# Performance work log

Measured on AMD Instinct MI355X. Metric: run time of the kernel, lower is better.

Reference implementation:

```python
import jax, jax.numpy as jnp
import numpy as np

NEG_SLOPE = 0.2
N_GRAPHS = 32

def gat_conv(x, src, dst, W, attn_l, attn_r, bias):
    """DGL-style GATConv: returns [N, H, D]."""
    H, D = attn_l.shape
    N = x.shape[0]
    feat = (x @ W).reshape(N, H, D)                     # [N,H,D]
    el = jnp.sum(feat * attn_l[None], axis=-1)          # [N,H]
    er = jnp.sum(feat * attn_r[None], axis=-1)          # [N,H]
    e = jax.nn.leaky_relu(el[src] + er[dst], NEG_SLOPE) # [E,H]
    # edge softmax over incoming edges of each dst node
    emax = jax.ops.segment_max(e, dst, num_segments=N)
    emax = jnp.where(jnp.isfinite(emax), emax, 0.0)     # zero in-degree guard
    ex = jnp.exp(e - emax[dst])
    den = jax.ops.segment_sum(ex, dst, num_segments=N)
    alpha = ex / jnp.maximum(den[dst], 1e-9)            # [E,H]
    msg = alpha[:, :, None] * feat[src]                 # [E,H,D]
    rst = jax.ops.segment_sum(msg, dst, num_segments=N) # [N,H,D]
    return rst + bias.reshape(1, H, D)

def branch(x, src, dst, gid, W1, al1, ar1, b1, W2, al2, ar2, b2):
    h = jax.nn.relu(gat_conv(x, src, dst, W1, al1, ar1, b1))  # [N,10,64]
    h = h.sum(axis=1)                                          # [N,64]
    h = jax.nn.relu(gat_conv(h, src, dst, W2, al2, ar2, b2))  # [N,1,128]
    h = h[:, 0, :]                                             # [N,128]
    g = jax.ops.segment_max(h, gid, num_segments=N_GRAPHS)     # [B,128] max readout
    return jnp.where(jnp.isfinite(g), g, 0.0)

def reference(lig_x, lig_src, lig_dst, lig_gid, rec_x, rec_src, rec_dst, rec_gid,
              W1l, al1l, ar1l, b1l, W2l, al2l, ar2l, b2l,
              W1r, al1r, ar1r, b1r, W2r, al2r, ar2r, b2r,
              Wlin1, blin1, Wlin2, blin2):
    hlig = branch(lig_x, lig_src, lig_dst, lig_gid, W1l, al1l, ar1l, b1l, W2l, al2l, ar2l, b2l)
    hrec = branch(rec_x, rec_src, rec_dst, rec_gid, W1r, al1r, ar1r, b1r, W2r, al2r, ar2r, b2r)
    h = jnp.concatenate([hlig, hrec], axis=1)           # [B,256]
    h = jax.nn.relu(h @ Wlin1 + blin1)
    h = jax.nn.relu(h @ Wlin2 + blin2)
    return h.reshape(-1)

def setup_inputs() -> dict:
    key = jax.random.key(0)
    ks = jax.random.split(key, 24)
    Nl, El, Nr, Er = 20000, 160000, 40000, 400000
    d = {}
    d['lig_x'] = jax.random.normal(ks[0], (Nl, 64), jnp.float32)
    d['lig_src'] = jax.random.randint(ks[1], (El,), 0, Nl, jnp.int32)
    d['lig_dst'] = jax.random.randint(ks[2], (El,), 0, Nl, jnp.int32)
    d['lig_gid'] = jnp.sort(jax.random.randint(ks[3], (Nl,), 0, N_GRAPHS, jnp.int32))
    d['rec_x'] = jax.random.normal(ks[4], (Nr, 64), jnp.float32)
    d['rec_src'] = jax.random.randint(ks[5], (Er,), 0, Nr, jnp.int32)
    d['rec_dst'] = jax.random.randint(ks[6], (Er,), 0, Nr, jnp.int32)
    d['rec_gid'] = jnp.sort(jax.random.randint(ks[7], (Nr,), 0, N_GRAPHS, jnp.int32))
    s = 0.1
    d['W1l'] = jax.random.normal(ks[8], (64, 640), jnp.float32) * s
    d['al1l'] = jax.random.normal(ks[9], (10, 64), jnp.float32) * s
    d['ar1l'] = jax.random.normal(ks[10], (10, 64), jnp.float32) * s
    d['b1l'] = jnp.zeros((640,), jnp.float32)
    d['W2l'] = jax.random.normal(ks[11], (64, 128), jnp.float32) * s
    d['al2l'] = jax.random.normal(ks[12], (1, 128), jnp.float32) * s
    d['ar2l'] = jax.random.normal(ks[13], (1, 128), jnp.float32) * s
    d['b2l'] = jnp.zeros((128,), jnp.float32)
    d['W1r'] = jax.random.normal(ks[14], (64, 640), jnp.float32) * s
    d['al1r'] = jax.random.normal(ks[15], (10, 64), jnp.float32) * s
    d['ar1r'] = jax.random.normal(ks[16], (10, 64), jnp.float32) * s
    d['b1r'] = jnp.zeros((640,), jnp.float32)
    d['W2r'] = jax.random.normal(ks[17], (64, 128), jnp.float32) * s
    d['al2r'] = jax.random.normal(ks[18], (1, 128), jnp.float32) * s
    d['ar2r'] = jax.random.normal(ks[19], (1, 128), jnp.float32) * s
    d['b2r'] = jnp.zeros((128,), jnp.float32)
    d['Wlin1'] = jax.random.normal(ks[20], (256, 128), jnp.float32) * s
    d['blin1'] = jnp.zeros((128,), jnp.float32)
    d['Wlin2'] = jax.random.normal(ks[21], (128, 1), jnp.float32) * s
    d['blin2'] = jnp.zeros((1,), jnp.float32)
    return d
```

## Files before the change

kernel.cpp:

```cpp
#include <hip/hip_runtime.h>
#include <hip/hip_bf16.h>

typedef short bf16x8 __attribute__((ext_vector_type(8)));
typedef float f32x4 __attribute__((ext_vector_type(4)));

__device__ inline float lrelu(float x) { return x > 0.f ? x : 0.2f * x; }

__device__ inline unsigned short f2bf(float f) {
    unsigned u = __float_as_uint(f);
    u = u + 0x7FFFu + ((u >> 16) & 1u);
    return (unsigned short)(u >> 16);
}

__global__ void init_misc(const float4* __restrict__ xl, int nl4,
                          const float4* __restrict__ xr, int nr4,
                          float4* __restrict__ xcat, int* __restrict__ deg,
                          const int* __restrict__ gidL, const int* __restrict__ gidR,
                          int* __restrict__ gs, int Nl, int Nr) {
    int Nc = Nl + Nr;
    int stride = gridDim.x * blockDim.x;
    int tid = blockIdx.x * blockDim.x + threadIdx.x;
    for (int i = tid; i < nl4 + nr4; i += stride)
        xcat[i] = (i < nl4) ? xl[i] : xr[i - nl4];
    for (int i = tid; i < Nc; i += stride) deg[i] = 0;
    for (int n = tid; n < Nc; n += stride) {
        if (n < Nl) {
            int gcur = gidL[n];
            int gprev = (n == 0) ? -1 : gidL[n - 1];
            for (int g = gprev + 1; g <= gcur; ++g) gs[g] = n;
            if (n == Nl - 1)
                for (int g = gcur + 1; g <= 32; ++g) gs[g] = Nl;
        } else {
            int ln = n - Nl;
            int gcur = gidR[ln];
            int gprev = (ln == 0) ? -1 : gidR[ln - 1];
            for (int g = gprev + 1; g <= gcur; ++g) gs[33 + g] = n;
            if (ln == Nr - 1)
                for (int g = gcur + 1; g <= 32; ++g) gs[33 + g] = Nc;
        }
    }
}

__global__ void fold_all(const float* __restrict__ W1l, const float* __restrict__ al1l,
                         const float* __restrict__ ar1l, float* __restrict__ o1l,
                         const float* __restrict__ W1r, const float* __restrict__ al1r,
                         const float* __restrict__ ar1r, float* __restrict__ o1r,
                         const float* __restrict__ W2l, const float* __restrict__ al2l,
                         const float* __restrict__ ar2l, float* __restrict__ o2l,
                         const float* __restrict__ W2r, const float* __restrict__ al2r,
                         const float* __restrict__ ar2r, float* __restrict__ o2r) {
    const float *W, *al, *ar;
    float* o;
    int H, D;
    switch (blockIdx.y) {
        case 0: W = W1l; al = al1l; ar = ar1l; o = o1l; H = 10; D = 64; break;
        case 1: W = W1r; al = al1r; ar = ar1r; o = o1r; H = 10; D = 64; break;
        case 2: W = W2l; al = al2l; ar = ar2l; o = o2l; H = 1; D = 128; break;
        default: W = W2r; al = al2r; ar = ar2r; o = o2r; H = 1; D = 128; break;
    }
    int k = blockIdx.x;
    int lane = threadIdx.x;
    int C = H * D;
    for (int h = 0; h < H; ++h) {
        float sl = 0.f, sr = 0.f;
        for (int d = lane; d < D; d += 64) {
            float w = W[(size_t)k * C + h * D + d];
            sl += w * al[h * D + d];
            sr += w * ar[h * D + d];
        }
        for (int off = 32; off; off >>= 1) {
            sl += __shfl_down(sl, off);
            sr += __shfl_down(sr, off);
        }
        if (lane == 0) {
            o[k * 2 * H + h] = sl;
            o[k * 2 * H + H + h] = sr;
        }
    }
}

__global__ void prep_walr_all(const float* __restrict__ w1l, const float* __restrict__ w1r,
                              const float* __restrict__ w2l, const float* __restrict__ w2r,
                              unsigned short* __restrict__ f1l, unsigned short* __restrict__ f1r,
                              unsigned short* __restrict__ f2l, unsigned short* __restrict__ f2r) {
    int stride = gridDim.x * blockDim.x;
    for (int idx0 = blockIdx.x * blockDim.x + threadIdx.x; idx0 < 6144; idx0 += stride) {
        const float* Walr;
        unsigned short* F;
        int C2, idx;
        if (idx0 < 2048)      { Walr = w1l; F = f1l; C2 = 20; idx = idx0; }
        else if (idx0 < 4096) { Walr = w1r; F = f1r; C2 = 20; idx = idx0 - 2048; }
        else if (idx0 < 5120) { Walr = w2l; F = f2l; C2 = 2;  idx = idx0 - 4096; }
        else                  { Walr = w2r; F = f2r; C2 = 2;  idx = idx0 - 5120; }
        int j = idx & 7;
        int lane = (idx >> 3) & 63;
        int step = (idx >> 9) & 1;
        int CT = idx >> 10;
        int k = ((lane >> 4) << 3) + j + (step << 5);
        int col = (CT << 4) + (lane & 15);
        F[idx] = (col < C2) ? f2bf(Walr[k * C2 + col]) : 0;
    }
}

__global__ void wfrag_all(const float* __restrict__ W1l, const float* __restrict__ W1r,
                          const float* __restrict__ W2l, const float* __restrict__ W2r,
                          unsigned short* __restrict__ f1l, unsigned short* __restrict__ f1r,
                          unsigned short* __restrict__ f2l, unsigned short* __restrict__ f2r) {
    int stride = gridDim.x * blockDim.x;
    for (int idx0 = blockIdx.x * blockDim.x + threadIdx.x; idx0 < 98304; idx0 += stride) {
        const float* W;
        unsigned short* F;
        int C, idx;
        if (idx0 < 40960)      { W = W1l; F = f1l; C = 640; idx = idx0; }
        else if (idx0 < 81920) { W = W1r; F = f1r; C = 640; idx = idx0 - 40960; }
        else if (idx0 < 90112) { W = W2l; F = f2l; C = 128; idx = idx0 - 81920; }
        else                   { W = W2r; F = f2r; C = 128; idx = idx0 - 90112; }
        int j = idx & 7;
        int lane = (idx >> 3) & 63;
        int step = (idx >> 9) & 1;
        int CT = idx >> 10;
        int k = ((lane >> 4) << 3) + j + (step << 5);
        int col = (CT << 4) + (lane & 15);
        F[idx] = f2bf(W[(size_t)k * C + col]);
    }
}

template <int H>
__global__ __launch_bounds__(256) void attn_mfma2(const float* __restrict__ x,
                                                  const bf16x8* __restrict__ Wfl,
                                                  const bf16x8* __restrict__ Wfr,
                                                  float* __restrict__ el,
                                                  float* __restrict__ er,
                                                  int Nl, int Nc, int nbl) {
    const int NCT = (2 * H + 15) / 16;
    int lane = threadIdx.x & 63;
    int w = threadIdx.x >> 6;
    int b = blockIdx.x;
    const bf16x8* Wf;
    int row0, rend_;
    if (b < nbl) { Wf = Wfl; row0 = b * 64 + w * 16; rend_ = Nl; }
    else         { Wf = Wfr; row0 = Nl + (b - nbl) * 64 + w * 16; rend_ = Nc; }
    int arow = row0 + (lane & 15);
    if (arow > rend_ - 1) arow = rend_ - 1;
    int kb = (lane >> 4) * 8;
    int colL = lane & 15;

    const float* xr = x + (size_t)arow * 64 + kb;
    float4 a0 = *reinterpret_cast<const float4*>(xr);
    float4 a1 = *reinterpret_cast<const float4*>(xr + 4);
    float4 a2 = *reinterpret_cast<const float4*>(xr + 32);
    float4 a3 = *reinterpret_cast<const float4*>(xr + 36);
    bf16x8 A0, A1;
    A0[0] = (short)f2bf(a0.x); A0[1] = (short)f2bf(a0.y);
    A0[2] = (short)f2bf(a0.z); A0[3] = (short)f2bf(a0.w);
    A0[4] = (short)f2bf(a1.x); A0[5] = (short)f2bf(a1.y);
    A0[6] = (short)f2bf(a1.z); A0[7] = (short)f2bf(a1.w);
    A1[0] = (short)f2bf(a2.x); A1[1] = (short)f2bf(a2.y);
    A1[2] = (short)f2bf(a2.z); A1[3] = (short)f2bf(a2.w);
    A1[4] = (short)f2bf(a3.x); A1[5] = (short)f2bf(a3.y);
    A1[6] = (short)f2bf(a3.z); A1[7] = (short)f2bf(a3.w);

    int rbase = row0 + (lane >> 4) * 4;
#pragma unroll
    for (int ct = 0; ct < NCT; ++ct) {
        bf16x8 B0 = Wf[(ct * 2 + 0) * 64 + lane];
        bf16x8 B1 = Wf[(ct * 2 + 1) * 64 + lane];
        f32x4 acc = {0, 0, 0, 0};
        acc = __builtin_amdgcn_mfma_f32_16x16x32_bf16(A0, B0, acc, 0, 0, 0);
        acc = __builtin_amdgcn_mfma_f32_16x16x32_bf16(A1, B1, acc, 0, 0, 0);
        int col = ct * 16 + colL;
#pragma unroll
        for (int r = 0; r < 4; ++r) {
            int row = rbase + r;
            if (row < rend_) {
                if (col < H) el[(size_t)row * H + col] = acc[r];
                else if (col < 2 * H) er[(size_t)row * H + col - H] = acc[r];
            }
        }
    }
}

__global__ void count_deg2(const int* __restrict__ dl, const int* __restrict__ dr,
                           int* __restrict__ deg, int El, int Er, int Nl) {
    int total = El + Er;
    int stride = gridDim.x * blockDim.x;
    for (int i = blockIdx.x * blockDim.x + threadIdx.x; i < total; i += stride) {
        int d = (i < El) ? dl[i] : (dr[i - El] + Nl);
        atomicAdd(&deg[d], 1);
    }
}

__global__ __launch_bounds__(256) void scan_local(const int* __restrict__ deg,
                                                  int* __restrict__ rowptr,
                                                  int* __restrict__ bsum, int N) {
    __shared__ int wsum[4];
    int t = threadIdx.x;
    int base = blockIdx.x * 2048 + t * 8;
    int v[8];
    int s = 0;
#pragma unroll
    for (int i = 0; i < 8; ++i) {
        int idx = base + i;
        v[i] = (idx < N) ? deg[idx] : 0;
        s += v[i];
    }
    int lane = t & 63, w = t >> 6;
    int incl = s;
    for (int off = 1; off < 64; off <<= 1) {
        int o = __shfl_up(incl, off);
        if (lane >= off) incl += o;
    }
    if (lane == 63) wsum[w] = incl;
    __syncthreads();
    int woff = 0;
    for (int i = 0; i < w; ++i) woff += wsum[i];
    int run = woff + incl - s;
#pragma unroll
    for (int i = 0; i < 8; ++i) {
        int idx = base + i;
        if (idx < N) rowptr[idx] = run;
        run += v[i];
    }
    if (t == 255) bsum[blockIdx.x] = woff + incl;
}

__global__ void scan_bsum(int* __restrict__ bsum, int* __restrict__ rowptrN, int nb) {
    int t = threadIdx.x;
    int v = (t < nb) ? bsum[t] : 0;
    int incl = v;
    for (int off = 1; off < 64; off <<= 1) {
        int o = __shfl_up(incl, off);
        if (t >= off) incl += o;
    }
    if (t < nb) bsum[t] = incl - v;
    if (t == 63) *rowptrN = incl;
}

__global__ __launch_bounds__(256) void scan_add_fused(int* __restrict__ rowptr,
                                                      const int* __restrict__ bsum,
                                                      const int* __restrict__ deg,
                                                      int* __restrict__ cursor,
                                                      int* __restrict__ dslot, int N) {
    int off = bsum[blockIdx.x];
    int base = blockIdx.x * 2048 + threadIdx.x * 8;
#pragma unroll
    for (int i = 0; i < 8; ++i) {
        int idx = base + i;
        if (idx < N) {
            int rp = rowptr[idx] + off;
            rowptr[idx] = rp;
            cursor[idx] = rp;
            int dg = deg[idx];
            for (int j = rp; j < rp + dg; ++j) dslot[j] = idx;
        }
    }
}

__global__ void fill_adj2(const int* __restrict__ sl, const int* __restrict__ dl,
                          const int* __restrict__ sr, const int* __restrict__ dr,
                          int* __restrict__ cursor, int* __restrict__ adj,
                          int El, int Er, int Nl) {
    int total = El + Er;
    int stride = gridDim.x * blockDim.x;
    for (int i = blockIdx.x * blockDim.x + threadIdx.x; i < total; i += stride) {
        int s, d;
        if (i < El) { s = sl[i]; d = dl[i]; }
        else        { s = sr[i - El] + Nl; d = dr[i - El] + Nl; }
        int pos = atomicAdd(&cursor[d], 1);
        adj[pos] = s;
    }
}

template <int H>
__global__ void edge_e(const int* __restrict__ adj, const int* __restrict__ dslot,
                       const float* __restrict__ el, const float* __restrict__ er,
                       float* __restrict__ e, int E) {
    int stride = gridDim.x * blockDim.x;
    for (int i = blockIdx.x * blockDim.x + threadIdx.x; i < E; i += stride) {
        int s = adj[i], d = dslot[i];
        const float* els = el + (size_t)s * H;
        const float* erd = er + (size_t)d * H;
#pragma unroll
        for (int h = 0; h < H; ++h)
            e[(size_t)i * H + h] = lrelu(els[h] + erd[h]);
    }
}

template <int H>
__global__ void node_norm(const int* __restrict__ rowptr, const float* __restrict__ e,
                          float* __restrict__ alpha, int N) {
    int stride = gridDim.x * blockDim.x;
    for (int n = blockIdx.x * blockDim.x + threadIdx.x; n < N; n += stride) {
        int rbeg = rowptr[n], rend = rowptr[n + 1];
        if (rbeg == rend) continue;
        float m[H], den[H];
#pragma unroll
        for (int h = 0; h < H; ++h) { m[h] = -INFINITY; den[h] = 0.f; }
        for (int j = rbeg; j < rend; ++j) {
#pragma unroll
            for (int h = 0; h < H; ++h) {
                float ev = e[(size_t)j * H + h];
                float newm = fmaxf(m[h], ev);
                den[h] = den[h] * __expf(m[h] - newm) + __expf(ev - newm);
                m[h] = newm;
            }
        }
        float inv[H];
#pragma unroll
        for (int h = 0; h < H; ++h) inv[h] = 1.f / fmaxf(den[h], 1e-9f);
        for (int j = rbeg; j < rend; ++j) {
#pragma unroll
            for (int h = 0; h < H; ++h)
                alpha[(size_t)j * H + h] = __expf(e[(size_t)j * H + h] - m[h]) * inv[h];
        }
    }
}

template <int H>
__global__ __launch_bounds__(256, 8) void gather_z_b(
        const int* __restrict__ rowptr, const int* __restrict__ adj,
        const float* __restrict__ alpha, const float* __restrict__ x,
        unsigned short* __restrict__ z, int N) {
    int lane = threadIdx.x & 63;
    int w = threadIdx.x >> 6;
    int wpb = blockDim.x >> 6;
    int wstride = gridDim.x * wpb;
    for (int n = blockIdx.x * wpb + w; n < N; n += wstride) {
        int rbeg = __builtin_amdgcn_readfirstlane(rowptr[n]);
        int rend = __builtin_amdgcn_readfirstlane(rowptr[n + 1]);
        float acc[H];
#pragma unroll
        for (int h = 0; h < H; ++h) acc[h] = 0.f;
        for (int base = rbeg; base < rend; base += 64) {
            int cnt = rend - base; if (cnt > 64) cnt = 64;
            int sv = adj[base + ((lane < cnt) ? lane : 0)];
            int j = 0;
            for (; j + 4 <= cnt; j += 4) {
                int s0 = __shfl(sv, j);
                int s1 = __shfl(sv, j + 1);
                int s2 = __shfl(sv, j + 2);
                int s3 = __shfl(sv, j + 3);
                float x0 = x[(size_t)s0 * 64 + lane];
                float x1 = x[(size_t)s1 * 64 + lane];
                float x2 = x[(size_t)s2 * 64 + lane];
                float x3 = x[(size_t)s3 * 64 + lane];
                const float* a0 = alpha + (size_t)(base + j) * H;
                const float* a1 = a0 + H;
                const float* a2 = a1 + H;
                const float* a3 = a2 + H;
#pragma unroll
                for (int h = 0; h < H; ++h)
                    acc[h] += a0[h] * x0 + a1[h] * x1 + a2[h] * x2 + a3[h] * x3;
            }
            for (; j < cnt; ++j) {
                int s = __shfl(sv, j);
                float xv = x[(size_t)s * 64 + lane];
                const float* al = alpha + (size_t)(base + j) * H;
#pragma unroll
                for (int h = 0; h < H; ++h) acc[h] += al[h] * xv;
            }
        }
#pragma unroll
        for (int h = 0; h < H; ++h)
            z[(size_t)n * (H * 64) + h * 64 + lane] = f2bf(acc[h]);
    }
}

template <int H>
__global__ __launch_bounds__(256) void gemm_heads2(
        const unsigned short* __restrict__ z, const bf16x8* __restrict__ Wfl,
        const bf16x8* __restrict__ Wfr, const float* __restrict__ bl,
        const float* __restrict__ br, float* __restrict__ out,
        int Nl, int Nc, int nbl) {
    const int SA = H * 64;
    int lane = threadIdx.x & 63;
    int w = threadIdx.x >> 6;
    int b = blockIdx.x;
    const bf16x8* Wf;
    const float* bias;
    int row0, rend_;
    if (b < nbl) { Wf = Wfl; bias = bl; row0 = b * 64 + w * 16; rend_ = Nl; }
    else         { Wf = Wfr; bias = br; row0 = Nl + (b - nbl) * 64 + w * 16; rend_ = Nc; }
    int arow = row0 + (lane & 15);
    if (arow > rend_ - 1) arow = rend_ - 1;
    int kb = (lane >> 4) * 8;
    int colL = lane & 15;

    f32x4 o0 = {0,0,0,0}, o1 = {0,0,0,0}, o2 = {0,0,0,0}, o3 = {0,0,0,0};

    for (int h = 0; h < H; ++h) {
        const unsigned short* zr = z + (size_t)arow * SA + h * 64 + kb;
        bf16x8 A0 = *reinterpret_cast<const bf16x8*>(zr);
        bf16x8 A1 = *reinterpret_cast<const bf16x8*>(zr + 32);

        f32x4 acc0 = {0,0,0,0}, acc1 = {0,0,0,0}, acc2 = {0,0,0,0}, acc3 = {0,0,0,0};
#define CT_STEP(accv, ct)                                                            \
        {                                                                            \
            bf16x8 B0 = Wf[((h * 4 + (ct)) * 2 + 0) * 64 + lane];                    \
            bf16x8 B1 = Wf[((h * 4 + (ct)) * 2 + 1) * 64 + lane];                    \
            accv = __builtin_amdgcn_mfma_f32_16x16x32_bf16(A0, B0, accv, 0, 0, 0);   \
            accv = __builtin_amdgcn_mfma_f32_16x16x32_bf16(A1, B1, accv, 0, 0, 0);   \
        }
        CT_STEP(acc0, 0) CT_STEP(acc1, 1) CT_STEP(acc2, 2) CT_STEP(acc3, 3)
#undef CT_STEP

#define EPI(ov, accv, ct)                                                            \
        {                                                                            \
            float bv = bias[h * 64 + (ct) * 16 + colL];                              \
            ov[0] += fmaxf(accv[0] + bv, 0.f);                                       \
            ov[1] += fmaxf(accv[1] + bv, 0.f);                                       \
            ov[2] += fmaxf(accv[2] + bv, 0.f);                                       \
            ov[3] += fmaxf(accv[3] + bv, 0.f);                                       \
        }
        EPI(o0, acc0, 0) EPI(o1, acc1, 1) EPI(o2, acc2, 2) EPI(o3, acc3, 3)
#undef EPI
    }

    int rbase = row0 + (lane >> 4) * 4;
#define ST(ov, ct)                                                                   \
    {                                                                                \
        _Pragma("unroll")                                                            \
        for (int r = 0; r < 4; ++r) {                                                \
            int row = rbase + r;                                                     \
            if (row < rend_) out[(size_t)row * 64 + (ct) * 16 + colL] = ov[r];       \
        }                                                                            \
    }
    ST(o0, 0) ST(o1, 1) ST(o2, 2) ST(o3, 3)
#undef ST
}

__global__ __launch_bounds__(256) void gemm_relu2(
        const unsigned short* __restrict__ z, const bf16x8* __restrict__ Wfl,
        const bf16x8* __restrict__ Wfr, const float* __restrict__ bl,
        const float* __restrict__ br, float* __restrict__ out,
        int Nl, int Nc, int nbl) {
    int lane = threadIdx.x & 63;
    int w = threadIdx.x >> 6;
    int b = blockIdx.x;
    const bf16x8* Wf;
    const float* bias;
    int row0, rend_;
    if (b < nbl) { Wf = Wfl; bias = bl; row0 = b * 64 + w * 16; rend_ = Nl; }
    else         { Wf = Wfr; bias = br; row0 = Nl + (b - nbl) * 64 + w * 16; rend_ = Nc; }
    int arow = row0 + (lane & 15);
    if (arow > rend_ - 1) arow = rend_ - 1;
    int kb = (lane >> 4) * 8;
    int colL = lane & 15;

    const unsigned short* zr = z + (size_t)arow * 64 + kb;
    bf16x8 A0 = *reinterpret_cast<const bf16x8*>(zr);
    bf16x8 A1 = *reinterpret_cast<const bf16x8*>(zr + 32);

    int rbase = row0 + (lane >> 4) * 4;
#define DO_CT(ct)                                                                    \
    {                                                                                \
        bf16x8 B0 = Wf[((ct) * 2 + 0) * 64 + lane];                                  \
        bf16x8 B1 = Wf[((ct) * 2 + 1) * 64 + lane];                                  \
        f32x4 acc = {0, 0, 0, 0};                                                    \
        acc = __builtin_amdgcn_mfma_f32_16x16x32_bf16(A0, B0, acc, 0, 0, 0);         \
        acc = __builtin_amdgcn_mfma_f32_16x16x32_bf16(A1, B1, acc, 0, 0, 0);         \
        float bv = bias[(ct) * 16 + colL];                                           \
        _Pragma("unroll")                                                            \
        for (int r = 0; r < 4; ++r) {                                                \
            int row = rbase + r;                                                     \
            if (row < rend_)                                                         \
                out[(size_t)row * 128 + (ct) * 16 + colL] = fmaxf(acc[r] + bv, 0.f); \
        }                                                                            \
    }
    DO_CT(0) DO_CT(1) DO_CT(2) DO_CT(3) DO_CT(4) DO_CT(5) DO_CT(6) DO_CT(7)
#undef DO_CT
}

__global__ __launch_bounds__(128) void graph_max2(const float* __restrict__ rst2,
                                                  const int* __restrict__ gstart,
                                                  float* __restrict__ gm) {
    int g = blockIdx.x;
    int b = g >> 5, gl = g & 31;
    int sp = blockIdx.y;
    int t = threadIdx.x;
    const int* gs = gstart + 33 * b;
    int rb = gs[gl], re = gs[gl + 1];
    float m = -INFINITY;
    for (int r = rb + sp; r < re; r += 8)
        m = fmaxf(m, rst2[(size_t)r * 128 + t]);
    gm[(size_t)((b * 8 + sp) * 32 + gl) * 128 + t] = m;
}

__global__ __launch_bounds__(256) void mlp_head2(
        const float* __restrict__ gml, const float* __restrict__ gmr,
        const float* __restrict__ W1, const float* __restrict__ b1,
        const float* __restrict__ W2, const float* __restrict__ b2,
        float* __restrict__ out) {
    __shared__ float hcat[256];
    __shared__ float part[256];
    __shared__ float h[128];
    int g = blockIdx.x;
    int t = threadIdx.x;
    {
        const float* gsrc = (t < 128) ? gml : gmr;
        int c = t & 127;
        float m = -INFINITY;
#pragma unroll
        for (int sp = 0; sp < 8; ++sp) m = fmaxf(m, gsrc[sp * 4096 + g * 128 + c]);
        hcat[t < 128 ? c : 128 + c] = fmaxf(m, 0.f);
    }
    __syncthreads();
    {
        int c = t & 127;
        int k0 = (t >> 7) << 7;
        float acc = 0.f;
#pragma unroll 4
        for (int k = 0; k < 128; ++k)
            acc += hcat[k0 + k] * W1[(size_t)(k0 + k) * 128 + c];
        part[t] = acc;
    }
    __syncthreads();
    if (t < 128) h[t] = fmaxf(part[t] + part[t + 128] + b1[t], 0.f);
    __syncthreads();
    if (t < 128) {
        float v = h[t] * W2[t];
        for (int off = 32; off; off >>= 1) v += __shfl_down(v, off);
        if ((t & 63) == 0) part[t >> 6] = v;
    }
    __syncthreads();
    if (t == 0) out[g] = fmaxf(part[0] + part[1] + b2[0], 0.f);
}

static inline unsigned nblk_elem(long long total) {
    long long b = (total + 255) / 256;
    if (b > 65535) b = 65535;
    if (b < 1) b = 1;
    return (unsigned)b;
}
static inline unsigned nblk_gather(long long nodes) {
    long long b = (nodes + 3) / 4;
    if (b > 65535) b = 65535;
    if (b < 1) b = 1;
    return (unsigned)b;
}

extern "C" void kernel_launch(void* const* d_in, const int* in_sizes, int n_in,
                              void* d_out, int out_size, void* d_ws, size_t ws_size,
                              hipStream_t stream) {
    const float* lig_x = (const float*)d_in[0];
    const int* lig_src = (const int*)d_in[1];
    const int* lig_dst = (const int*)d_in[2];
    const int* lig_gid = (const int*)d_in[3];
    const float* rec_x = (const float*)d_in[4];
    const int* rec_src = (const int*)d_in[5];
    const int* rec_dst = (const int*)d_in[6];
    const int* rec_gid = (const int*)d_in[7];
    const float* W1l = (const float*)d_in[8];
    const float* al1l = (const float*)d_in[9];
    const float* ar1l = (const float*)d_in[10];
    const float* b1l = (const float*)d_in[11];
    const float* W2l = (const float*)d_in[12];
    const float* al2l = (const float*)d_in[13];
    const float* ar2l = (const float*)d_in[14];
    const float* b2l = (const float*)d_in[15];
    const float* W1r = (const float*)d_in[16];
    const float* al1r = (const float*)d_in[17];
    const float* ar1r = (const float*)d_in[18];
    const float* b1r = (const float*)d_in[19];
    const float* W2r = (const float*)d_in[20];
    const float* al2r = (const float*)d_in[21];
    const float* ar2r = (const float*)d_in[22];
    const float* b2r = (const float*)d_in[23];
    const float* Wlin1 = (const float*)d_in[24];
    const float* blin1 = (const float*)d_in[25];
    const float* Wlin2 = (const float*)d_in[26];
    const float* blin2 = (const float*)d_in[27];

    int Nl = in_sizes[0] / 64, El = in_sizes[1];
    int Nr = in_sizes[4] / 64, Er = in_sizes[5];
    int Nc = Nl + Nr;
    int Ec = El + Er;
    int nbl = (Nl + 63) / 64;
    int nbr = (Nr + 63) / 64;

    char* ws = (char*)d_ws;
    float* xcat = (float*)ws;        ws += (size_t)Nc * 64 * 4;
    unsigned short* zb = (unsigned short*)ws;   ws += (size_t)Nc * 640 * 2;
    unsigned short* z2b = (unsigned short*)ws;  ws += (size_t)Nc * 64 * 2;
    float* h1 = (float*)ws;          ws += (size_t)Nc * 64 * 4;
    float* rst2 = (float*)ws;        ws += (size_t)Nc * 128 * 4;
    float* elb = (float*)ws;         ws += (size_t)Nc * 10 * 4;
    float* erb = (float*)ws;         ws += (size_t)Nc * 10 * 4;
    int* deg = (int*)ws;             ws += (size_t)Nc * 4;
    int* cursor = (int*)ws;          ws += (size_t)Nc * 4;
    int* rowptr = (int*)ws;          ws += (size_t)(Nc + 1) * 4;
    int* adj = (int*)ws;             ws += (size_t)Ec * 4;
    int* dslot = (int*)ws;           ws += (size_t)Ec * 4;
    float* ebuf = (float*)ws;        ws += (size_t)Ec * 10 * 4;
    float* alpha = (float*)ws;       ws += (size_t)Ec * 10 * 4;
    float* gm = (float*)ws;          ws += 2 * 8 * 32 * 128 * 4;
    int* gstart = (int*)ws;          ws += 66 * 4;
    int* bsum = (int*)ws;            ws += 64 * 4;
    float* walr1l = (float*)ws;      ws += 64 * 20 * 4;
    float* walr1r = (float*)ws;      ws += 64 * 20 * 4;
    float* walr2l = (float*)ws;      ws += 64 * 2 * 4;
    float* walr2r = (float*)ws;      ws += 64 * 2 * 4;
    unsigned short* wf1l = (unsigned short*)ws;  ws += 40960 * 2;
    unsigned short* wf1r = (unsigned short*)ws;  ws += 40960 * 2;
    unsigned short* wf2l = (unsigned short*)ws;  ws += 8192 * 2;
    unsigned short* wf2r = (unsigned short*)ws;  ws += 8192 * 2;
    unsigned short* wfa1l = (unsigned short*)ws; ws += 2048 * 2;
    unsigned short* wfa1r = (unsigned short*)ws; ws += 2048 * 2;
    unsigned short* wfa2l = (unsigned short*)ws; ws += 1024 * 2;
    unsigned short* wfa2r = (unsigned short*)ws; ws += 1024 * 2;

    int nb = (Nc + 2047) / 2048;

    wfrag_all<<<96, 256, 0, stream>>>(W1l, W1r, W2l, W2r, wf1l, wf1r, wf2l, wf2r);
    fold_all<<<dim3(64, 4), 64, 0, stream>>>(W1l, al1l, ar1l, walr1l,
                                             W1r, al1r, ar1r, walr1r,
                                             W2l, al2l, ar2l, walr2l,
                                             W2r, al2r, ar2r, walr2r);
    prep_walr_all<<<24, 256, 0, stream>>>(walr1l, walr1r, walr2l, walr2r,
                                          wfa1l, wfa1r, wfa2l, wfa2r);

    init_misc<<<nblk_elem((long long)Nc * 16), 256, 0, stream>>>(
        (const float4*)lig_x, Nl * 16, (const float4*)rec_x, Nr * 16, (float4*)xcat,
        deg, lig_gid, rec_gid, gstart, Nl, Nr);
    count_deg2<<<nblk_elem(Ec), 256, 0, stream>>>(lig_dst, rec_dst, deg, El, Er, Nl);
    scan_local<<<nb, 256, 0, stream>>>(deg, rowptr, bsum, Nc);
    scan_bsum<<<1, 64, 0, stream>>>(bsum, rowptr + Nc, nb);
    scan_add_fused<<<nb, 256, 0, stream>>>(rowptr, bsum, deg, cursor, dslot, Nc);
    fill_adj2<<<nblk_elem(Ec), 256, 0, stream>>>(lig_src, lig_dst, rec_src, rec_dst,
                                                 cursor, adj, El, Er, Nl);

    attn_mfma2<10><<<nbl + nbr, 256, 0, stream>>>(xcat, (const bf16x8*)wfa1l,
                                                  (const bf16x8*)wfa1r, elb, erb,
                                                  Nl, Nc, nbl);
    edge_e<10><<<nblk_elem(Ec), 256, 0, stream>>>(adj, dslot, elb, erb, ebuf, Ec);
    node_norm<10><<<nblk_elem(Nc), 256, 0, stream>>>(rowptr, ebuf, alpha, Nc);
    gather_z_b<10><<<nblk_gather(Nc), 256, 0, stream>>>(rowptr, adj, alpha, xcat, zb, Nc);
    gemm_heads2<10><<<nbl + nbr, 256, 0, stream>>>(zb, (const bf16x8*)wf1l,
                                                   (const bf16x8*)wf1r, b1l, b1r,
                                                   h1, Nl, Nc, nbl);

    attn_mfma2<1><<<nbl + nbr, 256, 0, stream>>>(h1, (const bf16x8*)wfa2l,
                                                 (const bf16x8*)wfa2r, elb, erb,
                                                 Nl, Nc, nbl);
    edge_e<1><<<nblk_elem(Ec), 256, 0, stream>>>(adj, dslot, elb, erb, ebuf, Ec);
    node_norm<1><<<nblk_elem(Nc), 256, 0, stream>>>(rowptr, ebuf, alpha, Nc);
    gather_z_b<1><<<nblk_gather(Nc), 256, 0, stream>>>(rowptr, adj, alpha, h1, z2b, Nc);
    gemm_relu2<<<nbl + nbr, 256, 0, stream>>>(z2b, (const bf16x8*)wf2l,
                                              (const bf16x8*)wf2r, b2l, b2r,
                                              rst2, Nl, Nc, nbl);
    graph_max2<<<dim3(64, 8), 128, 0, stream>>>(rst2, gstart, gm);
    mlp_head2<<<32, 256, 0, stream>>>(gm, gm + 8 * 32 * 128, Wlin1, blin1, Wlin2, blin2,
                                      (float*)d_out);
}
```

Measured before the change: 302.3 us.

## Fuse edge scores and online softmax into the gather kernel

Removes the separate edge_e and node_norm kernels and the dslot, ebuf and alpha buffers. Each wavefront now computes its node's edge logits, an online-softmax max and denominator through wave shuffles, and the weighted sum in a single pass, normalising once at the end. This cuts several large per-edge intermediate writes and reads plus four kernel launches. In exchange it adds many shuffles and extra register pressure for H=10, which is why the minimum-waves launch bound is lowered to 4.

```diff
diff --git a/kernel.cpp b/kernel.cpp
--- a/kernel.cpp
+++ b/kernel.cpp
@@ -238,9 +238,7 @@
 
 __global__ __launch_bounds__(256) void scan_add_fused(int* __restrict__ rowptr,
                                                       const int* __restrict__ bsum,
-                                                      const int* __restrict__ deg,
-                                                      int* __restrict__ cursor,
-                                                      int* __restrict__ dslot, int N) {
+                                                      int* __restrict__ cursor, int N) {
     int off = bsum[blockIdx.x];
     int base = blockIdx.x * 2048 + threadIdx.x * 8;
 #pragma unroll
@@ -250,8 +248,6 @@
             int rp = rowptr[idx] + off;
             rowptr[idx] = rp;
             cursor[idx] = rp;
-            int dg = deg[idx];
-            for (int j = rp; j < rp + dg; ++j) dslot[j] = idx;
         }
     }
 }
@@ -271,56 +267,11 @@
     }
 }
 
-template <int H>
-__global__ void edge_e(const int* __restrict__ adj, const int* __restrict__ dslot,
-                       const float* __restrict__ el, const float* __restrict__ er,
-                       float* __restrict__ e, int E) {
-    int stride = gridDim.x * blockDim.x;
-    for (int i = blockIdx.x * blockDim.x + threadIdx.x; i < E; i += stride) {
-        int s = adj[i], d = dslot[i];
-        const float* els = el + (size_t)s * H;
-        const float* erd = er + (size_t)d * H;
-#pragma unroll
-        for (int h = 0; h < H; ++h)
-            e[(size_t)i * H + h] = lrelu(els[h] + erd[h]);
-    }
-}
-
-template <int H>
-__global__ void node_norm(const int* __restrict__ rowptr, const float* __restrict__ e,
-                          float* __restrict__ alpha, int N) {
-    int stride = gridDim.x * blockDim.x;
-    for (int n = blockIdx.x * blockDim.x + threadIdx.x; n < N; n += stride) {
-        int rbeg = rowptr[n], rend = rowptr[n + 1];
-        if (rbeg == rend) continue;
-        float m[H], den[H];
-#pragma unroll
-        for (int h = 0; h < H; ++h) { m[h] = -INFINITY; den[h] = 0.f; }
-        for (int j = rbeg; j < rend; ++j) {
-#pragma unroll
-            for (int h = 0; h < H; ++h) {
-                float ev = e[(size_t)j * H + h];
-                float newm = fmaxf(m[h], ev);
-                den[h] = den[h] * __expf(m[h] - newm) + __expf(ev - newm);
-                m[h] = newm;
-            }
-        }
-        float inv[H];
-#pragma unroll
-        for (int h = 0; h < H; ++h) inv[h] = 1.f / fmaxf(den[h], 1e-9f);
-        for (int j = rbeg; j < rend; ++j) {
-#pragma unroll
-            for (int h = 0; h < H; ++h)
-                alpha[(size_t)j * H + h] = __expf(e[(size_t)j * H + h] - m[h]) * inv[h];
-        }
-    }
-}
-
-template <int H>
-__global__ __launch_bounds__(256, 8) void gather_z_b(
+template <int H, int MINW>
+__global__ __launch_bounds__(256, MINW) void gather_fused(
         const int* __restrict__ rowptr, const int* __restrict__ adj,
-        const float* __restrict__ alpha, const float* __restrict__ x,
-        unsigned short* __restrict__ z, int N) {
+        const float* __restrict__ el, const float* __restrict__ er,
+        const float* __restrict__ x, unsigned short* __restrict__ z, int N) {
     int lane = threadIdx.x & 63;
     int w = threadIdx.x >> 6;
     int wpb = blockDim.x >> 6;
@@ -328,12 +279,39 @@
     for (int n = blockIdx.x * wpb + w; n < N; n += wstride) {
         int rbeg = __builtin_amdgcn_readfirstlane(rowptr[n]);
         int rend = __builtin_amdgcn_readfirstlane(rowptr[n + 1]);
-        float acc[H];
-#pragma unroll
-        for (int h = 0; h < H; ++h) acc[h] = 0.f;
+        float erh[H], mrun[H], den[H], acc[H];
+#pragma unroll
+        for (int h = 0; h < H; ++h) {
+            erh[h] = er[(size_t)n * H + h];
+            mrun[h] = -INFINITY;
+            den[h] = 0.f;
+            acc[h] = 0.f;
+        }
         for (int base = rbeg; base < rend; base += 64) {
             int cnt = rend - base; if (cnt > 64) cnt = 64;
             int sv = adj[base + ((lane < cnt) ? lane : 0)];
+            float ex[H];
+            {
+                const float* els = el + (size_t)sv * H;
+#pragma unroll
+                for (int h = 0; h < H; ++h)
+                    ex[h] = (lane < cnt) ? lrelu(els[h] + erh[h]) : -INFINITY;
+            }
+#pragma unroll
+            for (int h = 0; h < H; ++h) {
+                float cm = ex[h];
+                for (int off = 32; off; off >>= 1) cm = fmaxf(cm, __shfl_xor(cm, off));
+                float newm = fmaxf(mrun[h], cm);
+                float scl = __expf(mrun[h] - newm);
+                den[h] *= scl;
+                acc[h] *= scl;
+                mrun[h] = newm;
+                float e = (lane < cnt) ? __expf(ex[h] - newm) : 0.f;
+                float sm = e;
+                for (int off = 32; off; off >>= 1) sm += __shfl_xor(sm, off);
+                den[h] += sm;
+                ex[h] = e;
+            }
             int j = 0;
             for (; j + 4 <= cnt; j += 4) {
                 int s0 = __shfl(sv, j);
@@ -344,25 +322,23 @@
                 float x1 = x[(size_t)s1 * 64 + lane];
                 float x2 = x[(size_t)s2 * 64 + lane];
                 float x3 = x[(size_t)s3 * 64 + lane];
-                const float* a0 = alpha + (size_t)(base + j) * H;
-                const float* a1 = a0 + H;
-                const float* a2 = a1 + H;
-                const float* a3 = a2 + H;
 #pragma unroll
                 for (int h = 0; h < H; ++h)
-                    acc[h] += a0[h] * x0 + a1[h] * x1 + a2[h] * x2 + a3[h] * x3;
+                    acc[h] += __shfl(ex[h], j) * x0 + __shfl(ex[h], j + 1) * x1 +
+                              __shfl(ex[h], j + 2) * x2 + __shfl(ex[h], j + 3) * x3;
             }
             for (; j < cnt; ++j) {
                 int s = __shfl(sv, j);
                 float xv = x[(size_t)s * 64 + lane];
-                const float* al = alpha + (size_t)(base + j) * H;
-#pragma unroll
-                for (int h = 0; h < H; ++h) acc[h] += al[h] * xv;
+#pragma unroll
+                for (int h = 0; h < H; ++h) acc[h] += __shfl(ex[h], j) * xv;
             }
         }
 #pragma unroll
-        for (int h = 0; h < H; ++h)
-            z[(size_t)n * (H * 64) + h * 64 + lane] = f2bf(acc[h]);
+        for (int h = 0; h < H; ++h) {
+            float inv = 1.f / fmaxf(den[h], 1e-9f);
+            z[(size_t)n * (H * 64) + h * 64 + lane] = f2bf(acc[h] * inv);
+        }
     }
 }
 
@@ -590,9 +566,6 @@
     int* cursor = (int*)ws;          ws += (size_t)Nc * 4;
     int* rowptr = (int*)ws;          ws += (size_t)(Nc + 1) * 4;
     int* adj = (int*)ws;             ws += (size_t)Ec * 4;
-    int* dslot = (int*)ws;           ws += (size_t)Ec * 4;
-    float* ebuf = (float*)ws;        ws += (size_t)Ec * 10 * 4;
-    float* alpha = (float*)ws;       ws += (size_t)Ec * 10 * 4;
     float* gm = (float*)ws;          ws += 2 * 8 * 32 * 128 * 4;
     int* gstart = (int*)ws;          ws += 66 * 4;
     int* bsum = (int*)ws;            ws += 64 * 4;
@@ -625,16 +598,15 @@
     count_deg2<<<nblk_elem(Ec), 256, 0, stream>>>(lig_dst, rec_dst, deg, El, Er, Nl);
     scan_local<<<nb, 256, 0, stream>>>(deg, rowptr, bsum, Nc);
     scan_bsum<<<1, 64, 0, stream>>>(bsum, rowptr + Nc, nb);
-    scan_add_fused<<<nb, 256, 0, stream>>>(rowptr, bsum, deg, cursor, dslot, Nc);
+    scan_add_fused<<<nb, 256, 0, stream>>>(rowptr, bsum, cursor, Nc);
     fill_adj2<<<nblk_elem(Ec), 256, 0, stream>>>(lig_src, lig_dst, rec_src, rec_dst,
                                                  cursor, adj, El, Er, Nl);
 
     attn_mfma2<10><<<nbl + nbr, 256, 0, stream>>>(xcat, (const bf16x8*)wfa1l,
                                                   (const bf16x8*)wfa1r, elb, erb,
                                                   Nl, Nc, nbl);
-    edge_e<10><<<nblk_elem(Ec), 256, 0, stream>>>(adj, dslot, elb, erb, ebuf, Ec);
-    node_norm<10><<<nblk_elem(Nc), 256, 0, stream>>>(rowptr, ebuf, alpha, Nc);
-    gather_z_b<10><<<nblk_gather(Nc), 256, 0, stream>>>(rowptr, adj, alpha, xcat, zb, Nc);
+    gather_fused<10, 4><<<nblk_gather(Nc), 256, 0, stream>>>(rowptr, adj, elb, erb,
+                                                             xcat, zb, Nc);
     gemm_heads2<10><<<nbl + nbr, 256, 0, stream>>>(zb, (const bf16x8*)wf1l,
                                                    (const bf16x8*)wf1r, b1l, b1r,
                                                    h1, Nl, Nc, nbl);
@@ -642,9 +614,8 @@
     attn_mfma2<1><<<nbl + nbr, 256, 0, stream>>>(h1, (const bf16x8*)wfa2l,
                                                  (const bf16x8*)wfa2r, elb, erb,
                                                  Nl, Nc, nbl);
-    edge_e<1><<<nblk_elem(Ec), 256, 0, stream>>>(adj, dslot, elb, erb, ebuf, Ec);
-    node_norm<1><<<nblk_elem(Nc), 256, 0, stream>>>(rowptr, ebuf, alpha, Nc);
-    gather_z_b<1><<<nblk_gather(Nc), 256, 0, stream>>>(rowptr, adj, alpha, h1, z2b, Nc);
+    gather_fused<1, 8><<<nblk_gather(Nc), 256, 0, stream>>>(rowptr, adj, elb, erb,
+                                                            h1, z2b, Nc);
     gemm_relu2<<<nbl + nbr, 256, 0, stream>>>(z2b, (const bf16x8*)wf2l,
                                               (const bf16x8*)wf2r, b2l, b2r,
                                               rst2, Nl, Nc, nbl);
```

Result: slower. 359.4 us (+18.9%).
